# Kernel optimization log

Hardware: AMD Instinct MI355X
Metric: run time of the kernel (lower is better)

## Reference

```python
import jax, jax.numpy as jnp
import numpy as np

B_, L_, H_, N_ = 8, 1024, 1024, 64

def setup_inputs() -> dict:
    key = jax.random.key(0)
    k1, k2, k3, k4 = jax.random.split(key, 4)
    return {
        "samples": jax.random.normal(k1, (B_, L_, 3 * H_), dtype=jnp.float32),
        "label_one_hot": jax.random.uniform(k2, (B_, L_, N_), dtype=jnp.float32),
        "predict": jax.random.normal(k3, (B_, L_, N_), dtype=jnp.float32),
        "W": jax.random.normal(k4, (H_, 3 * H_), dtype=jnp.float32) * (1.0 / np.sqrt(3 * H_)),
        "b_proj": jnp.zeros((H_,), dtype=jnp.float32),
    }

def reference(samples, label_one_hot, predict, W, b_proj):
    # projection: Linear(3H -> H)
    s = jnp.einsum("blk,hk->blh", samples, W) + b_proj          # [b,L,H]
    # dense similarity graph with diagonal masked out, row-softmax
    graph = jnp.einsum("blh,bmh->blm", s, s)                     # [b,L,L]
    L = graph.shape[1]
    eye = jnp.eye(L, dtype=graph.dtype)
    A = jax.nn.softmax(graph - 1e5 * eye, axis=-1)               # [b,L,L]
    # centered masked labels
    sup = label_one_hot
    row_has = (jnp.sum(sup, axis=-1) > 0.5).astype(sup.dtype)    # [b,L]
    total = jnp.sum(row_has, axis=-1)[:, None]                   # [b,1]
    avg = (jnp.sum(sup, axis=-2) / total)[:, None, :]            # [b,1,N]
    B0 = (sup - avg) * row_has[..., None]                        # [b,L,N]
    # diagonal inverse-degree scaling (elementwise, no dense diag matmul)
    d = 1.0 / (jnp.sum(A, axis=-1) + 1e-10)                      # [b,L]
    P = d[:, :, None] * jnp.swapaxes(A, -1, -2)                  # [b,L,L]
    Db = d[:, :, None] * B0                                      # [b,L,N]
    # 6-step power-iteration scan with residual injection at t==3
    ut = jnp.zeros_like(B0)
    for t in range(1, 7):
        ut = jnp.einsum("blm,bmn->bln", P, ut) + Db
        if t == 3:
            ut = ut + predict  # dropout is identity in eval mode
    return ut

if __name__ == "__main__":
    out = reference(**setup_inputs())
    print(out.shape, out.dtype)
```

## Files before the change

kernel.cpp:

```cpp
#include <hip/hip_runtime.h>


typedef _Float16 f16_t;
typedef f16_t f16x4 __attribute__((ext_vector_type(4)));
typedef f16_t f16x8 __attribute__((ext_vector_type(8)));
typedef float floatx4 __attribute__((ext_vector_type(4)));

__device__ __forceinline__ void async_copy16(const void* g, void* l) {
  __builtin_amdgcn_global_load_lds(
      (const __attribute__((address_space(1))) void*)g,
      (__attribute__((address_space(3))) void*)l, 16, 0, 0);
}

__device__ __forceinline__ f16_t hi_of(float x) { return (f16_t)x; }
__device__ __forceinline__ f16_t lo_of(float x, f16_t h) {
  return (f16_t)(x - (float)h);
}

__global__ __launch_bounds__(256) void prep_kernel(
    const float* __restrict__ W, f16_t* __restrict__ Whi, f16_t* __restrict__ Wlo,
    const float* __restrict__ samples, f16_t* __restrict__ SampH)
{
  const int bx = blockIdx.x, tid = threadIdx.x;
  if (bx < 3072) {
    const int i = bx * 256 + tid;
    float4 v = ((const float4*)W)[i];
    v.x *= 32.f; v.y *= 32.f; v.z *= 32.f; v.w *= 32.f;
    f16x4 h, l;
    f16_t h0 = hi_of(v.x); h[0] = h0; l[0] = lo_of(v.x, h0);
    f16_t h1 = hi_of(v.y); h[1] = h1; l[1] = lo_of(v.y, h1);
    f16_t h2 = hi_of(v.z); h[2] = h2; l[2] = lo_of(v.z, h2);
    f16_t h3 = hi_of(v.w); h[3] = h3; l[3] = lo_of(v.w, h3);
    *(f16x4*)(Whi + (size_t)i * 4) = h;
    *(f16x4*)(Wlo + (size_t)i * 4) = l;
  } else {
    const int i = (bx - 3072) * 256 + tid;
    const float4 v = ((const float4*)samples)[i];
    f16x4 h;
    h[0] = (f16_t)v.x; h[1] = (f16_t)v.y; h[2] = (f16_t)v.z; h[3] = (f16_t)v.w;
    *(f16x4*)(SampH + (size_t)i * 4) = h;
  }
}

template <int CMODE>
__global__ __launch_bounds__(256) void gemm_mfma(
    const f16_t* __restrict__ AhiG,
    const f16_t* __restrict__ BhiG, const f16_t* __restrict__ BloG,
    const float* __restrict__ bias,
    float* __restrict__ Cf, f16_t* __restrict__ Chi, f16_t* __restrict__ Clo,
    int M, int N, int K, long long sA, long long sB, long long sC, float cscale)
{
  AhiG += (long long)blockIdx.z * sA;
  BhiG += (long long)blockIdx.z * sB;
  BloG += (long long)blockIdx.z * sB;
  if (CMODE == 1) Cf += (long long)blockIdx.z * sC;

  __shared__ __align__(16) f16_t AsHi[2 * 128 * 32];
  __shared__ __align__(16) f16_t BsHi[2 * 128 * 32];
  __shared__ __align__(16) f16_t BsLo[2 * 128 * 32];

  const int tid = threadIdx.x;
  const int lane = tid & 63;
  const int wave = tid >> 6;
  const int wm = wave >> 1, wn = wave & 1;
  const int m0 = blockIdx.y * 128;
  const int n0 = blockIdx.x * 128;

  const int fr = lane & 15;
  const int kg = (lane >> 4) * 8;
  const int aoff = (wm * 64 + fr) * 32 + kg;
  const int boff = (wn * 64 + fr) * 32 + kg;

  floatx4 acc[4][4] = {};

  for (int k0 = 0; k0 < K; k0 += 64) {
    __syncthreads();
#pragma unroll
    for (int it = 0; it < 4; ++it) {
      const int cb = it * 256 + wave * 64;
      const int c = cb + lane;
      const int kk = c >> 9;
      const int row = (c >> 2) & 127;
      const int kc = kk * 32 + (c & 3) * 8;
      const size_t ga = (size_t)(m0 + row) * K + k0 + kc;
      const size_t gb = (size_t)(n0 + row) * K + k0 + kc;
      async_copy16(AhiG + ga, (char*)AsHi + (size_t)cb * 16);
      async_copy16(BhiG + gb, (char*)BsHi + (size_t)cb * 16);
      async_copy16(BloG + gb, (char*)BsLo + (size_t)cb * 16);
    }
    __syncthreads();

#pragma unroll
    for (int kk = 0; kk < 2; ++kk) {
      f16x8 ah[4], bh[4], bl[4];
#pragma unroll
      for (int t = 0; t < 4; ++t) {
        ah[t] = *(const f16x8*)&AsHi[kk * 4096 + aoff + t * 512];
        bh[t] = *(const f16x8*)&BsHi[kk * 4096 + boff + t * 512];
        bl[t] = *(const f16x8*)&BsLo[kk * 4096 + boff + t * 512];
      }
#pragma unroll
      for (int i = 0; i < 4; ++i)
#pragma unroll
        for (int j = 0; j < 4; ++j) {
          acc[i][j] = __builtin_amdgcn_mfma_f32_16x16x32_f16(ah[i], bh[j], acc[i][j], 0, 0, 0);
          acc[i][j] = __builtin_amdgcn_mfma_f32_16x16x32_f16(ah[i], bl[j], acc[i][j], 0, 0, 0);
        }
    }
  }

  const int mr = (lane >> 4) * 4;
#pragma unroll
  for (int j = 0; j < 4; ++j) {
    const int n = n0 + wn * 64 + j * 16 + fr;
    const float bj = (CMODE == 0) ? bias[n] : 0.f;
#pragma unroll
    for (int i = 0; i < 4; ++i) {
#pragma unroll
      for (int r = 0; r < 4; ++r) {
        const int m = m0 + wm * 64 + i * 16 + mr + r;
        float v = acc[i][j][r];
        if (CMODE == 0) {
          v = v * cscale + bj;
          f16_t h = hi_of(v);
          Chi[(size_t)m * N + n] = h;
          Clo[(size_t)m * N + n] = lo_of(v, h);
        } else {
          if (m == n) v -= 1e5f;
          Cf[(size_t)m * N + n] = v;
        }
      }
    }
  }
}

__global__ __launch_bounds__(256) void rowstats_kernel(
    const float* __restrict__ G, float* __restrict__ mx, float* __restrict__ inv)
{
  __shared__ float red[4];
  const int tid = threadIdx.x;
  const float* g = G + (size_t)blockIdx.x * 1024;
  const float4 v = ((const float4*)g)[tid];

  float m = fmaxf(fmaxf(v.x, v.y), fmaxf(v.z, v.w));
#pragma unroll
  for (int off = 32; off > 0; off >>= 1) m = fmaxf(m, __shfl_down(m, off));
  if ((tid & 63) == 0) red[tid >> 6] = m;
  __syncthreads();
  m = fmaxf(fmaxf(red[0], red[1]), fmaxf(red[2], red[3]));
  __syncthreads();

  float s = __expf(v.x - m) + __expf(v.y - m) + __expf(v.z - m) + __expf(v.w - m);
#pragma unroll
  for (int off = 32; off > 0; off >>= 1) s += __shfl_down(s, off);
  if ((tid & 63) == 0) red[tid >> 6] = s;
  __syncthreads();
  if (tid == 0) {
    mx[blockIdx.x] = m;
    inv[blockIdx.x] = 1.0f / (red[0] + red[1] + red[2] + red[3]);
  }
}

__global__ __launch_bounds__(256) void make_at_kernel(
    const float* __restrict__ G, const float* __restrict__ mx,
    const float* __restrict__ inv, f16_t* __restrict__ At)
{
  const int row = blockIdx.x;
  const int b = row >> 10;
  const int tid = threadIdx.x;
  const float4 g = ((const float4*)(G + (size_t)row * 1024))[tid];
  const float4 m = ((const float4*)(mx + b * 1024))[tid];
  const float4 iv = ((const float4*)(inv + b * 1024))[tid];
  f16x4 o;
  o[0] = (f16_t)(__expf(g.x - m.x) * iv.x);
  o[1] = (f16_t)(__expf(g.y - m.y) * iv.y);
  o[2] = (f16_t)(__expf(g.z - m.z) * iv.z);
  o[3] = (f16_t)(__expf(g.w - m.w) * iv.w);
  *(f16x4*)(At + (size_t)row * 1024 + tid * 4) = o;
}

__global__ __launch_bounds__(1024) void make_db_kernel(
    const float* __restrict__ sup, float* __restrict__ Db, f16_t* __restrict__ DbT)
{
  const int L = 1024, Nn = 64;
  const float* s = sup + (size_t)blockIdx.x * L * Nn;
  float* db = Db + (size_t)blockIdx.x * L * Nn;
  f16_t* dbt = DbT + (size_t)blockIdx.x * L * Nn;
  __shared__ float rowhas[1024];
  __shared__ float cpart[1024];
  __shared__ float tpart[16];
  __shared__ float avg[64];
  __shared__ float totalsh;
  const int tid = threadIdx.x;

  const float4* sr = (const float4*)(s + (size_t)tid * 64);
  float ss = 0.f;
#pragma unroll
  for (int i = 0; i < 16; ++i) { const float4 v = sr[i]; ss += (v.x + v.y) + (v.z + v.w); }
  const float rh = (ss > 0.5f) ? 1.f : 0.f;
  rowhas[tid] = rh;
  float t = rh;
#pragma unroll
  for (int off = 32; off > 0; off >>= 1) t += __shfl_down(t, off);
  if ((tid & 63) == 0) tpart[tid >> 6] = t;

  const int n = tid & 63, seg = tid >> 6;
  float cs = 0.f;
  for (int l = seg * 64; l < seg * 64 + 64; ++l) cs += s[(size_t)l * 64 + n];
  cpart[seg * 64 + n] = cs;
  __syncthreads();
  if (tid == 0) { float tt = 0.f; for (int i = 0; i < 16; ++i) tt += tpart[i]; totalsh = tt; }
  __syncthreads();
  if (tid < 64) {
    float a = 0.f;
    for (int i = 0; i < 16; ++i) a += cpart[i * 64 + tid];
    avg[tid] = a / totalsh;
  }
  __syncthreads();

  const float4* s4 = (const float4*)s;
  float4* d4 = (float4*)db;
  for (int i = tid; i < (L * Nn) / 4; i += 1024) {
    float4 v = s4[i];
    const int l = i >> 4;
    const int nb = (i & 15) * 4;
    const float rhl = rowhas[l];
    v.x = (v.x - avg[nb + 0]) * rhl;
    v.y = (v.y - avg[nb + 1]) * rhl;
    v.z = (v.z - avg[nb + 2]) * rhl;
    v.w = (v.w - avg[nb + 3]) * rhl;
    d4[i] = v;
  }
  for (int i = tid; i < L * Nn; i += 1024) {
    const int n2 = i >> 10, l2 = i & 1023;
    dbt[i] = (f16_t)((s[(size_t)l2 * 64 + n2] - avg[n2]) * rowhas[l2]);
  }
}

__global__ __launch_bounds__(256) void iter_part(
    const f16_t* __restrict__ At, const f16_t* __restrict__ UT,
    float* __restrict__ Part)
{
  const int L = 1024, Nn = 64;
  const int b = blockIdx.y, l0 = blockIdx.x * 64, ks = blockIdx.z;
  At += (size_t)b * L * L;
  UT += (size_t)b * Nn * L;
  Part += (((size_t)ks * 8 + b) * L) * Nn;

  __shared__ __align__(16) f16_t AtS[2 * 64 * 32];
  __shared__ __align__(16) f16_t UtS[2 * 64 * 32];

  const int tid = threadIdx.x;
  const int lane = tid & 63;
  const int wave = tid >> 6;
  const int fr = lane & 15;
  const int kg = (lane >> 4) * 8;

  floatx4 acc[4] = {};

  for (int mi = 0; mi < 4; ++mi) {
    const int m0 = ks * 256 + mi * 64;
    __syncthreads();
#pragma unroll
    for (int it = 0; it < 2; ++it) {
      const int cb = it * 256 + wave * 64;
      const int c = cb + lane;
      const int kk = c >> 8;
      const int row = (c >> 2) & 63;
      const int kc = kk * 32 + (c & 3) * 8;
      async_copy16(At + (size_t)(l0 + row) * L + m0 + kc, (char*)AtS + (size_t)cb * 16);
      async_copy16(UT + (size_t)row * L + m0 + kc, (char*)UtS + (size_t)cb * 16);
    }
    __syncthreads();
#pragma unroll
    for (int kk = 0; kk < 2; ++kk) {
      const f16x8 a = *(const f16x8*)&AtS[kk * 2048 + (wave * 16 + fr) * 32 + kg];
#pragma unroll
      for (int j = 0; j < 4; ++j) {
        const f16x8 bf = *(const f16x8*)&UtS[kk * 2048 + (j * 16 + fr) * 32 + kg];
        acc[j] = __builtin_amdgcn_mfma_f32_16x16x32_f16(a, bf, acc[j], 0, 0, 0);
      }
    }
  }

  const int mr = (lane >> 4) * 4;
#pragma unroll
  for (int j = 0; j < 4; ++j) {
    const int n = j * 16 + fr;
#pragma unroll
    for (int r = 0; r < 4; ++r) {
      const int l = wave * 16 + mr + r;
      Part[(size_t)(l0 + l) * Nn + n] = acc[j][r];
    }
  }
}

template <int PRED, int FINAL>
__global__ __launch_bounds__(256) void iter_fin(
    const float* __restrict__ Part, const float* __restrict__ Db,
    const float* __restrict__ Pred, f16_t* __restrict__ UTn,
    float* __restrict__ OutF)
{
  const int L = 1024, Nn = 64;
  const int b = blockIdx.y, l0 = blockIdx.x * 64;
  const size_t base = ((size_t)b * L + l0) * Nn;
  const size_t ksStride = (size_t)8 * L * Nn;
  Db += base;
  if (PRED) Pred += base;

  __shared__ f16_t OutS[64 * 72];
  const int tid = threadIdx.x;

#pragma unroll
  for (int it = 0; it < 4; ++it) {
    const int idx = it * 256 + tid;
    const int l = idx >> 4, n4 = (idx & 15) * 4;
    const size_t o = (size_t)l * Nn + n4;
    float4 v = *(const float4*)(Part + base + o);
    const float4 p1 = *(const float4*)(Part + base + ksStride + o);
    const float4 p2 = *(const float4*)(Part + base + 2 * ksStride + o);
    const float4 p3 = *(const float4*)(Part + base + 3 * ksStride + o);
    v.x += p1.x; v.y += p1.y; v.z += p1.z; v.w += p1.w;
    v.x += p2.x; v.y += p2.y; v.z += p2.z; v.w += p2.w;
    v.x += p3.x; v.y += p3.y; v.z += p3.z; v.w += p3.w;
    const float4 d = *(const float4*)(Db + o);
    v.x += d.x; v.y += d.y; v.z += d.z; v.w += d.w;
    if (PRED) {
      const float4 p = *(const float4*)(Pred + o);
      v.x += p.x; v.y += p.y; v.z += p.z; v.w += p.w;
    }
    if (FINAL) {
      *(float4*)(OutF + base + o) = v;
    } else {
      OutS[(n4 + 0) * 72 + l] = (f16_t)v.x;
      OutS[(n4 + 1) * 72 + l] = (f16_t)v.y;
      OutS[(n4 + 2) * 72 + l] = (f16_t)v.z;
      OutS[(n4 + 3) * 72 + l] = (f16_t)v.w;
    }
  }
  if (!FINAL) {
    __syncthreads();
    f16_t* dst = UTn + (size_t)b * Nn * L;
#pragma unroll
    for (int it = 0; it < 2; ++it) {
      const int c = it * 256 + tid;
      const int n = c >> 3, lc = (c & 7) * 8;
      *(f16x8*)(dst + (size_t)n * L + l0 + lc) = *(const f16x8*)&OutS[n * 72 + lc];
    }
  }
}

extern "C" void kernel_launch(void* const* d_in, const int* in_sizes, int n_in,
                              void* d_out, int out_size, void* d_ws, size_t ws_size,
                              hipStream_t stream) {
  const float* samples = (const float*)d_in[0];
  const float* label   = (const float*)d_in[1];
  const float* predict = (const float*)d_in[2];
  const float* W       = (const float*)d_in[3];
  const float* bproj   = (const float*)d_in[4];
  float* out = (float*)d_out;

  char* ws = (char*)d_ws;
  f16_t* Whi = (f16_t*)ws;
  f16_t* Wlo = (f16_t*)(ws + 6291456);
  float* mx  = (float*)ws;
  float* inv = (float*)(ws + 32768);
  float* Db  = (float*)(ws + 65536);
  f16_t* DbT = (f16_t*)(ws + 65536 + 2097152);
  f16_t* UTa = (f16_t*)(ws + 65536 + 3145728);
  f16_t* UTb = (f16_t*)(ws + 65536 + 4194304);
  f16_t* SampH = (f16_t*)(ws + 12582912);
  float* G     = (float*)(ws + 12582912);
  f16_t* Shi = (f16_t*)(ws + 62914560);
  f16_t* Slo = (f16_t*)(ws + 62914560 + 16777216);
  f16_t* At  = Shi;
  float* Part = (float*)Slo;

  const long long LH = 1024LL * 1024;
  const long long LL = 1024LL * 1024;

  prep_kernel<<<dim3(27648), 256, 0, stream>>>(W, Whi, Wlo, samples, SampH);

  gemm_mfma<0><<<dim3(8, 64, 1), 256, 0, stream>>>(
      SampH, Whi, Wlo, bproj, nullptr, Shi, Slo,
      8192, 1024, 3072, 0, 0, 0, 1.0f / 32.0f);

  gemm_mfma<1><<<dim3(8, 8, 8), 256, 0, stream>>>(
      Shi, Shi, Slo, nullptr, G, nullptr, nullptr,
      1024, 1024, 1024, LH, LH, LL, 1.0f);

  rowstats_kernel<<<8192, 256, 0, stream>>>(G, mx, inv);
  make_at_kernel<<<8192, 256, 0, stream>>>(G, mx, inv, At);

  make_db_kernel<<<8, 1024, 0, stream>>>(label, Db, DbT);

  dim3 gp(16, 8, 4), gf(16, 8);
  iter_part<<<gp, 256, 0, stream>>>(At, DbT, Part);
  iter_fin<0, 0><<<gf, 256, 0, stream>>>(Part, Db, nullptr, UTa, nullptr);
  iter_part<<<gp, 256, 0, stream>>>(At, UTa, Part);
  iter_fin<1, 0><<<gf, 256, 0, stream>>>(Part, Db, predict, UTb, nullptr);
  iter_part<<<gp, 256, 0, stream>>>(At, UTb, Part);
  iter_fin<0, 0><<<gf, 256, 0, stream>>>(Part, Db, nullptr, UTa, nullptr);
  iter_part<<<gp, 256, 0, stream>>>(At, UTa, Part);
  iter_fin<0, 0><<<gf, 256, 0, stream>>>(Part, Db, nullptr, UTb, nullptr);
  iter_part<<<gp, 256, 0, stream>>>(At, UTb, Part);
  iter_fin<0, 1><<<gf, 256, 0, stream>>>(Part, Db, nullptr, nullptr, out);
}
```

Baseline: 420.8 us.

## Fuse split-K partial reduction into next iteration's matmul prologue

Each power-iteration step now reduces the previous step's four split-K partials, adds Db and the optional predict residual, and writes its own 256-wide f16 U slice straight into shared memory. This replaces the separate finalize kernel and the transposed f16 U buffer in global memory. It removes four kernel launches and a global write/read round trip per step. In exchange, the reduction is done redundantly by the 16 row-blocks that share each k-slice, and the larger LDS footprint could lower occupancy. Ping-pong partial buffers are added so the step being computed does not overwrite partials it still reads.

```diff
diff --git a/kernel.cpp b/kernel.cpp
--- a/kernel.cpp
+++ b/kernel.cpp
@@ -237,24 +237,61 @@
   }
 }
 
-__global__ __launch_bounds__(256) void iter_part(
-    const f16_t* __restrict__ At, const f16_t* __restrict__ UT,
-    float* __restrict__ Part)
+template <int FIRST, int PRED>
+__global__ __launch_bounds__(256) void iter_step(
+    const f16_t* __restrict__ At, const f16_t* __restrict__ DbT,
+    const float* __restrict__ PartPrev, const float* __restrict__ Db,
+    const float* __restrict__ Pred, float* __restrict__ PartOut)
 {
   const int L = 1024, Nn = 64;
   const int b = blockIdx.y, l0 = blockIdx.x * 64, ks = blockIdx.z;
   At += (size_t)b * L * L;
-  UT += (size_t)b * Nn * L;
-  Part += (((size_t)ks * 8 + b) * L) * Nn;
+  PartOut += (((size_t)ks * 8 + b) * L) * Nn;
 
   __shared__ __align__(16) f16_t AtS[2 * 64 * 32];
-  __shared__ __align__(16) f16_t UtS[2 * 64 * 32];
+  __shared__ __align__(16) f16_t UtFull[64 * 264];
 
   const int tid = threadIdx.x;
   const int lane = tid & 63;
   const int wave = tid >> 6;
   const int fr = lane & 15;
   const int kg = (lane >> 4) * 8;
+
+  if (FIRST) {
+    const f16_t* dbt = DbT + (size_t)b * Nn * L + ks * 256;
+#pragma unroll
+    for (int it = 0; it < 8; ++it) {
+      const int idx = it * 256 + tid;
+      const int n = idx >> 5, lc = (idx & 31) * 8;
+      *(f16x8*)&UtFull[n * 264 + lc] = *(const f16x8*)(dbt + (size_t)n * L + lc);
+    }
+  } else {
+    const size_t base = ((size_t)b * L + ks * 256) * Nn;
+    const size_t ksS = (size_t)8 * L * Nn;
+#pragma unroll
+    for (int it = 0; it < 16; ++it) {
+      const int idx = it * 256 + tid;
+      const int lql = idx >> 4, n4 = (idx & 15) * 4;
+      const size_t o = base + (size_t)lql * Nn + n4;
+      float4 v = *(const float4*)(PartPrev + o);
+      const float4 p1 = *(const float4*)(PartPrev + o + ksS);
+      const float4 p2 = *(const float4*)(PartPrev + o + 2 * ksS);
+      const float4 p3 = *(const float4*)(PartPrev + o + 3 * ksS);
+      v.x += p1.x; v.y += p1.y; v.z += p1.z; v.w += p1.w;
+      v.x += p2.x; v.y += p2.y; v.z += p2.z; v.w += p2.w;
+      v.x += p3.x; v.y += p3.y; v.z += p3.z; v.w += p3.w;
+      const float4 d = *(const float4*)(Db + o);
+      v.x += d.x; v.y += d.y; v.z += d.z; v.w += d.w;
+      if (PRED) {
+        const float4 p = *(const float4*)(Pred + o);
+        v.x += p.x; v.y += p.y; v.z += p.z; v.w += p.w;
+      }
+      UtFull[(n4 + 0) * 264 + lql] = (f16_t)v.x;
+      UtFull[(n4 + 1) * 264 + lql] = (f16_t)v.y;
+      UtFull[(n4 + 2) * 264 + lql] = (f16_t)v.z;
+      UtFull[(n4 + 3) * 264 + lql] = (f16_t)v.w;
+    }
+  }
 
   floatx4 acc[4] = {};
 
@@ -269,15 +306,15 @@
       const int row = (c >> 2) & 63;
       const int kc = kk * 32 + (c & 3) * 8;
       async_copy16(At + (size_t)(l0 + row) * L + m0 + kc, (char*)AtS + (size_t)cb * 16);
-      async_copy16(UT + (size_t)row * L + m0 + kc, (char*)UtS + (size_t)cb * 16);
     }
     __syncthreads();
 #pragma unroll
     for (int kk = 0; kk < 2; ++kk) {
       const f16x8 a = *(const f16x8*)&AtS[kk * 2048 + (wave * 16 + fr) * 32 + kg];
+      const int uoff = mi * 64 + kk * 32 + kg;
 #pragma unroll
       for (int j = 0; j < 4; ++j) {
-        const f16x8 bf = *(const f16x8*)&UtS[kk * 2048 + (j * 16 + fr) * 32 + kg];
+        const f16x8 bf = *(const f16x8*)&UtFull[(j * 16 + fr) * 264 + uoff];
         acc[j] = __builtin_amdgcn_mfma_f32_16x16x32_f16(a, bf, acc[j], 0, 0, 0);
       }
     }
@@ -290,63 +327,36 @@
 #pragma unroll
     for (int r = 0; r < 4; ++r) {
       const int l = wave * 16 + mr + r;
-      Part[(size_t)(l0 + l) * Nn + n] = acc[j][r];
-    }
-  }
-}
-
-template <int PRED, int FINAL>
-__global__ __launch_bounds__(256) void iter_fin(
+      PartOut[(size_t)(l0 + l) * Nn + n] = acc[j][r];
+    }
+  }
+}
+
+__global__ __launch_bounds__(256) void final_fin(
     const float* __restrict__ Part, const float* __restrict__ Db,
-    const float* __restrict__ Pred, f16_t* __restrict__ UTn,
     float* __restrict__ OutF)
 {
   const int L = 1024, Nn = 64;
   const int b = blockIdx.y, l0 = blockIdx.x * 64;
   const size_t base = ((size_t)b * L + l0) * Nn;
-  const size_t ksStride = (size_t)8 * L * Nn;
-  Db += base;
-  if (PRED) Pred += base;
-
-  __shared__ f16_t OutS[64 * 72];
+  const size_t ksS = (size_t)8 * L * Nn;
   const int tid = threadIdx.x;
 
 #pragma unroll
   for (int it = 0; it < 4; ++it) {
     const int idx = it * 256 + tid;
     const int l = idx >> 4, n4 = (idx & 15) * 4;
-    const size_t o = (size_t)l * Nn + n4;
-    float4 v = *(const float4*)(Part + base + o);
-    const float4 p1 = *(const float4*)(Part + base + ksStride + o);
-    const float4 p2 = *(const float4*)(Part + base + 2 * ksStride + o);
-    const float4 p3 = *(const float4*)(Part + base + 3 * ksStride + o);
+    const size_t o = base + (size_t)l * Nn + n4;
+    float4 v = *(const float4*)(Part + o);
+    const float4 p1 = *(const float4*)(Part + o + ksS);
+    const float4 p2 = *(const float4*)(Part + o + 2 * ksS);
+    const float4 p3 = *(const float4*)(Part + o + 3 * ksS);
     v.x += p1.x; v.y += p1.y; v.z += p1.z; v.w += p1.w;
     v.x += p2.x; v.y += p2.y; v.z += p2.z; v.w += p2.w;
     v.x += p3.x; v.y += p3.y; v.z += p3.z; v.w += p3.w;
     const float4 d = *(const float4*)(Db + o);
     v.x += d.x; v.y += d.y; v.z += d.z; v.w += d.w;
-    if (PRED) {
-      const float4 p = *(const float4*)(Pred + o);
-      v.x += p.x; v.y += p.y; v.z += p.z; v.w += p.w;
-    }
-    if (FINAL) {
-      *(float4*)(OutF + base + o) = v;
-    } else {
-      OutS[(n4 + 0) * 72 + l] = (f16_t)v.x;
-      OutS[(n4 + 1) * 72 + l] = (f16_t)v.y;
-      OutS[(n4 + 2) * 72 + l] = (f16_t)v.z;
-      OutS[(n4 + 3) * 72 + l] = (f16_t)v.w;
-    }
-  }
-  if (!FINAL) {
-    __syncthreads();
-    f16_t* dst = UTn + (size_t)b * Nn * L;
-#pragma unroll
-    for (int it = 0; it < 2; ++it) {
-      const int c = it * 256 + tid;
-      const int n = c >> 3, lc = (c & 7) * 8;
-      *(f16x8*)(dst + (size_t)n * L + l0 + lc) = *(const f16x8*)&OutS[n * 72 + lc];
-    }
+    *(float4*)(OutF + o) = v;
   }
 }
 
@@ -367,14 +377,13 @@
   float* inv = (float*)(ws + 32768);
   float* Db  = (float*)(ws + 65536);
   f16_t* DbT = (f16_t*)(ws + 65536 + 2097152);
-  f16_t* UTa = (f16_t*)(ws + 65536 + 3145728);
-  f16_t* UTb = (f16_t*)(ws + 65536 + 4194304);
   f16_t* SampH = (f16_t*)(ws + 12582912);
   float* G     = (float*)(ws + 12582912);
   f16_t* Shi = (f16_t*)(ws + 62914560);
   f16_t* Slo = (f16_t*)(ws + 62914560 + 16777216);
   f16_t* At  = Shi;
-  float* Part = (float*)Slo;
+  float* PartA = (float*)Slo;
+  float* PartB = (float*)(ws + 62914560 + 16777216 + 8388608);
 
   const long long LH = 1024LL * 1024;
   const long long LL = 1024LL * 1024;
@@ -395,14 +404,10 @@
   make_db_kernel<<<8, 1024, 0, stream>>>(label, Db, DbT);
 
   dim3 gp(16, 8, 4), gf(16, 8);
-  iter_part<<<gp, 256, 0, stream>>>(At, DbT, Part);
-  iter_fin<0, 0><<<gf, 256, 0, stream>>>(Part, Db, nullptr, UTa, nullptr);
-  iter_part<<<gp, 256, 0, stream>>>(At, UTa, Part);
-  iter_fin<1, 0><<<gf, 256, 0, stream>>>(Part, Db, predict, UTb, nullptr);
-  iter_part<<<gp, 256, 0, stream>>>(At, UTb, Part);
-  iter_fin<0, 0><<<gf, 256, 0, stream>>>(Part, Db, nullptr, UTa, nullptr);
-  iter_part<<<gp, 256, 0, stream>>>(At, UTa, Part);
-  iter_fin<0, 0><<<gf, 256, 0, stream>>>(Part, Db, nullptr, UTb, nullptr);
-  iter_part<<<gp, 256, 0, stream>>>(At, UTb, Part);
-  iter_fin<0, 1><<<gf, 256, 0, stream>>>(Part, Db, nullptr, nullptr, out);
-}
+  iter_step<1, 0><<<gp, 256, 0, stream>>>(At, DbT, nullptr, Db, nullptr, PartA);
+  iter_step<0, 0><<<gp, 256, 0, stream>>>(At, nullptr, PartA, Db, nullptr, PartB);
+  iter_step<0, 1><<<gp, 256, 0, stream>>>(At, nullptr, PartB, Db, predict, PartA);
+  iter_step<0, 0><<<gp, 256, 0, stream>>>(At, nullptr, PartA, Db, nullptr, PartB);
+  iter_step<0, 0><<<gp, 256, 0, stream>>>(At, nullptr, PartB, Db, nullptr, PartA);
+  final_fin<<<gf, 256, 0, stream>>>(PartA, Db, out);
+}
```

Result: slower. 459.5 us (+9.2%).

## Exploit symmetry of Gram matrix: compute lower-triangular tiles and mirror via LDS transpose

Applied to the files above, without the earlier changes.

The S·S^T similarity GEMM now launches only the 36 lower-triangular 128x128 tiles per batch instead of all 64. Each off-diagonal tile writes its direct result and then stages the accumulator through shared memory to write the transposed tile as well. This aims to nearly halve the MFMA work of the second GEMM. In exchange it adds extra LDS staging, barriers and scalar transposed stores, and the off-diagonal tiles run longer.

```diff
diff --git a/kernel.cpp b/kernel.cpp
--- a/kernel.cpp
+++ b/kernel.cpp
@@ -55,16 +55,26 @@
   BloG += (long long)blockIdx.z * sB;
   if (CMODE == 1) Cf += (long long)blockIdx.z * sC;
 
-  __shared__ __align__(16) f16_t AsHi[2 * 128 * 32];
-  __shared__ __align__(16) f16_t BsHi[2 * 128 * 32];
-  __shared__ __align__(16) f16_t BsLo[2 * 128 * 32];
+  __shared__ __align__(16) char smem[49152];
+  f16_t* AsHi = (f16_t*)smem;
+  f16_t* BsHi = (f16_t*)(smem + 16384);
+  f16_t* BsLo = (f16_t*)(smem + 32768);
 
   const int tid = threadIdx.x;
   const int lane = tid & 63;
   const int wave = tid >> 6;
   const int wm = wave >> 1, wn = wave & 1;
-  const int m0 = blockIdx.y * 128;
-  const int n0 = blockIdx.x * 128;
+
+  int m0, n0;
+  if (CMODE == 0) {
+    m0 = blockIdx.y * 128;
+    n0 = blockIdx.x * 128;
+  } else {
+    int idx = blockIdx.x, i = 0, accu = 0;
+    while (accu + i + 1 <= idx) { accu += i + 1; ++i; }
+    m0 = i * 128;
+    n0 = (idx - accu) * 128;
+  }
 
   const int fr = lane & 15;
   const int kg = (lane >> 4) * 8;
@@ -130,6 +140,35 @@
           Cf[(size_t)m * N + n] = v;
         }
       }
+    }
+  }
+
+  if (CMODE == 1 && m0 != n0) {
+    float* T = (float*)smem;
+#pragma unroll
+    for (int mc = 0; mc < 4; ++mc) {
+      __syncthreads();
+      if (wm == (mc >> 1)) {
+        const int ibase = (mc & 1) * 2;
+#pragma unroll
+        for (int di = 0; di < 2; ++di) {
+#pragma unroll
+          for (int j = 0; j < 4; ++j) {
+            const int nl = wn * 64 + j * 16 + fr;
+#pragma unroll
+            for (int r = 0; r < 4; ++r) {
+              const int mloc = di * 16 + mr + r;
+              T[nl * 36 + mloc] = acc[ibase + di][j][r];
+            }
+          }
+        }
+      }
+      __syncthreads();
+      const int row = tid >> 1, half = tid & 1;
+      const float* src = &T[row * 36 + half * 16];
+      float* dst = Cf + (size_t)(n0 + row) * N + m0 + mc * 32 + half * 16;
+#pragma unroll
+      for (int q = 0; q < 16; ++q) dst[q] = src[q];
     }
   }
 }
@@ -385,7 +424,7 @@
       SampH, Whi, Wlo, bproj, nullptr, Shi, Slo,
       8192, 1024, 3072, 0, 0, 0, 1.0f / 32.0f);
 
-  gemm_mfma<1><<<dim3(8, 8, 8), 256, 0, stream>>>(
+  gemm_mfma<1><<<dim3(36, 1, 8), 256, 0, stream>>>(
       Shi, Shi, Slo, nullptr, G, nullptr, nullptr,
       1024, 1024, 1024, LH, LH, LL, 1.0f);
 
```

New measurement: 419.6 us. About the same (-0.3%).
